# Performance work log

Measured on AMD Instinct MI355X. Metric: run time of the kernel, lower is better.

Reference implementation:

```python
import jax, jax.numpy as jnp
import numpy as np

E_ENT = 50000   # entities
R_REL = 500     # relations (dual graph nodes)
N_EDGE = 500000 # triples
D = 256
HID = D // 2
ALPHA = 0.1
BETA = 0.3
SLOPE = 0.01    # torch F.leaky_relu default

def _leaky(x):
    return jnp.where(x > 0, x, SLOPE * x)

def _compute_r(X, head_r, tail_r):
    # mean head / tail entity embedding per relation -> [R, 2D]
    L = (head_r.T @ X) / head_r.sum(0)[:, None]
    Rm = (tail_r.T @ X) / tail_r.sum(0)[:, None]
    return jnp.concatenate([L, Rm], axis=-1)

def _dense_att(vals_in, feats, adj, w1, w2, b2, w3, b3):
    # conv1d(k=1) == linear; feats [R, 2D]
    in_fts = feats @ w1.T                # [R, HID]
    f1 = in_fts @ w2.T + b2              # [R, 1]
    f2 = in_fts @ w3.T + b3              # [R, 1]
    logits = adj * (f1 + f2.T)           # [R, R]
    bias = -1e9 * (1.0 - (adj > 0).astype(jnp.float32))
    coefs = jax.nn.softmax(_leaky(logits) + bias, axis=1)
    return jax.nn.relu(coefs @ vals_in)

def _sparse_att(X, dual_layer, row, col, rel, w, b):
    # per-relation scalar score, gathered per edge, sparse row-softmax, sparse mm
    score = (dual_layer @ w.T + b)[:, 0]          # [R]
    logit = _leaky(score[rel])                    # [E]
    m = jax.ops.segment_max(logit, row, num_segments=E_ENT)
    ex = jnp.exp(logit - m[row])
    s = jax.ops.segment_sum(ex, row, num_segments=E_ENT)
    coef = ex / s[row]
    out = jnp.zeros_like(X).at[row].add(coef[:, None] * X[col])
    return jax.nn.relu(out)

def _gcn(X, W, m_row, m_col, m_val):
    # sparse.mm(M, X * W); dropout omitted (eval mode)
    Xw = X * W
    out = jnp.zeros_like(X).at[m_row].add(m_val[:, None] * Xw[m_col])
    return jax.nn.relu(out)

def _highway(l1, l2, K, b):
    t = jax.nn.sigmoid(l1 @ K + b)
    return t * l2 + (1.0 - t) * l1

def setup_inputs() -> dict:
    key = jax.random.key(0)
    ks = jax.random.split(key, 24)
    e, r, ne, d, hid = E_ENT, R_REL, N_EDGE, D, HID
    u = lambda k, sh: jax.random.uniform(k, sh, dtype=jnp.float32)
    n = lambda k, sh: jax.random.normal(k, sh, dtype=jnp.float32)
    gl = lambda k, sh: n(k, sh) * (2.0 / (sh[0] + sh[-1])) ** 0.5
    return {
        'X0': n(ks[0], (e, d)) * 0.1,
        'head_r': u(ks[1], (e, r)),
        'tail_r': u(ks[2], (e, r)),
        'dual_A': u(ks[3], (r, r)),
        'edge_row': jax.random.randint(ks[4], (ne,), 0, e),
        'edge_col': jax.random.randint(ks[5], (ne,), 0, e),
        'edge_rel': jax.random.randint(ks[6], (ne,), 0, r),
        'm_row': jax.random.randint(ks[7], (ne,), 0, e),
        'm_col': jax.random.randint(ks[8], (ne,), 0, e),
        'm_val': u(ks[9], (ne,)) * 1e-1,
        'w_self1': gl(ks[10], (hid, 2 * d)),
        'w_self2': gl(ks[11], (1, hid)), 'b_self2': jnp.zeros((1,), jnp.float32),
        'w_self3': gl(ks[12], (1, hid)), 'b_self3': jnp.zeros((1,), jnp.float32),
        'w_sp1': gl(ks[13], (1, 2 * d)), 'b_sp1': jnp.zeros((1,), jnp.float32),
        'w_dual1': gl(ks[14], (hid, 2 * d)),
        'w_dual2': gl(ks[15], (1, hid)), 'b_dual2': jnp.zeros((1,), jnp.float32),
        'w_dual3': gl(ks[16], (1, hid)), 'b_dual3': jnp.zeros((1,), jnp.float32),
        'w_sp2': gl(ks[17], (1, 2 * d)), 'b_sp2': jnp.zeros((1,), jnp.float32),
        'w_gcn1': jnp.ones((1, d), jnp.float32),
        'w_gcn2': jnp.ones((1, d), jnp.float32),
        'k_hw1': gl(ks[18], (d, d)), 'bg_hw1': jnp.zeros((d,), jnp.float32),
        'k_hw2': gl(ks[19], (d, d)), 'bg_hw2': jnp.zeros((d,), jnp.float32),
    }

def reference(X0, head_r, tail_r, dual_A, edge_row, edge_col, edge_rel,
              m_row, m_col, m_val,
              w_self1, w_self2, b_self2, w_self3, b_self3, w_sp1, b_sp1,
              w_dual1, w_dual2, b_dual2, w_dual3, b_dual3, w_sp2, b_sp2,
              w_gcn1, w_gcn2, k_hw1, bg_hw1, k_hw2, bg_hw2):
    dX1 = _compute_r(X0, head_r, tail_r)
    dH1 = _dense_att(dX1, dX1, dual_A, w_self1, w_self2, b_self2, w_self3, b_self3)
    pH1 = _sparse_att(X0, dH1, edge_row, edge_col, edge_rel, w_sp1, b_sp1)
    pX1 = X0 + ALPHA * pH1
    dX2 = _compute_r(pX1, head_r, tail_r)
    dH2 = _dense_att(dH1, dX2, dual_A, w_dual1, w_dual2, b_dual2, w_dual3, b_dual3)
    pH2 = _sparse_att(pX1, dH2, edge_row, edge_col, edge_rel, w_sp2, b_sp2)
    pX2 = X0 + BETA * pH2
    g1 = _gcn(pX2, w_gcn1, m_row, m_col, m_val)
    h1 = _highway(pX2, g1, k_hw1, bg_hw1)
    g2 = _gcn(h1, w_gcn2, m_row, m_col, m_val)
    return _highway(h1, g2, k_hw2, bg_hw2)
```

## Files before the change

kernel.cpp:

```cpp
#include <hip/hip_runtime.h>
#include <stdint.h>

#define E_ENT 50000
#define R_REL 500
#define NEDGE 500000
#define DD 256
#define D2 512
#define KSPLIT 50
#define KCHUNK 1000

typedef unsigned short u16;
typedef unsigned int u32;
typedef __attribute__((ext_vector_type(8))) short bf16x8;
typedef __attribute__((ext_vector_type(4))) float f32x4;

__device__ __forceinline__ float bf2f(u16 u) {
  union { u32 i; float f; } v; v.i = ((u32)u) << 16; return v.f;
}
__device__ __forceinline__ u16 f2bf(float f) {
  union { float f; u32 i; } v; v.f = f;
  u32 r = v.i + 0x7fffu + ((v.i >> 16) & 1u);
  return (u16)(r >> 16);
}
__device__ __forceinline__ float lrelu(float x) { return x > 0.f ? x : 0.01f * x; }

__device__ __forceinline__ uint4 ld4g(const u16* p, bool v) {
  if (v) return *(const uint4*)p;
  return make_uint4(0u, 0u, 0u, 0u);
}
__device__ __forceinline__ float4 ldf4(const float* p, bool v) {
  if (v) return *(const float4*)p;
  return make_float4(0.f, 0.f, 0.f, 0.f);
}

__device__ __forceinline__ uint4 pk4(const float4& x, const float4& y) {
  uint4 r;
  r.x = (u32)f2bf(x.x) | ((u32)f2bf(x.y) << 16);
  r.y = (u32)f2bf(x.z) | ((u32)f2bf(x.w) << 16);
  r.z = (u32)f2bf(y.x) | ((u32)f2bf(y.y) << 16);
  r.w = (u32)f2bf(y.z) | ((u32)f2bf(y.w) << 16);
  return r;
}

__device__ __forceinline__ int lds_addr(int col, int e) {
  return col * 64 + ((((e >> 3) ^ col ^ (col >> 3)) & 7) << 3) + (e & 7);
}

__device__ __forceinline__ void pack_store(u16* __restrict__ lds, int colBase, int e,
                                           const uint4& x, const uint4& y) {
  const u32* xp = (const u32*)&x;
  const u32* yp = (const u32*)&y;
#pragma unroll
  for (int i = 0; i < 4; ++i) {
    u32 xv = xp[i], yv = yp[i];
    u32 lo = (xv & 0xffffu) | (yv << 16);
    u32 hi = (xv >> 16) | (yv & 0xffff0000u);
    int c0 = colBase + 2 * i;
    *(u32*)(lds + lds_addr(c0, e)) = lo;
    *(u32*)(lds + lds_addr(c0 + 1, e)) = hi;
  }
}

__global__ void k_cast(const float* __restrict__ in, u16* __restrict__ out, int n4) {
  int i = blockIdx.x * 256 + threadIdx.x;
  if (i < n4) {
    float4 v = *(const float4*)(in + (size_t)i * 4);
    uint2 o;
    o.x = (u32)f2bf(v.x) | ((u32)f2bf(v.y) << 16);
    o.y = (u32)f2bf(v.z) | ((u32)f2bf(v.w) << 16);
    *(uint2*)(out + (size_t)i * 4) = o;
  }
}

__global__ void k_hist(const int* __restrict__ rows, int* __restrict__ cnt) {
  int i = blockIdx.x * 256 + threadIdx.x;
  if (i < NEDGE) atomicAdd(&cnt[rows[i]], 1);
}

__global__ void k_bsum(const int* __restrict__ cnt, int* __restrict__ bsum) {
  __shared__ int sb[256];
  int t = threadIdx.x, i = blockIdx.x * 256 + t;
  sb[t] = (i < E_ENT) ? cnt[i] : 0;
  __syncthreads();
  for (int s = 128; s; s >>= 1) { if (t < s) sb[t] += sb[t + s]; __syncthreads(); }
  if (t == 0) bsum[blockIdx.x] = sb[0];
}

__global__ void k_scanb(const int* __restrict__ bsum, int* __restrict__ boff, int nb) {
  __shared__ int sb[256];
  int t = threadIdx.x;
  int v = (t < nb) ? bsum[t] : 0;
  sb[t] = v;
  __syncthreads();
  for (int o = 1; o < 256; o <<= 1) {
    int x = (t >= o) ? sb[t - o] : 0;
    __syncthreads();
    sb[t] += x;
    __syncthreads();
  }
  if (t < nb) boff[t] = sb[t] - v;
}

__global__ void k_apply(const int* __restrict__ cnt, const int* __restrict__ boff,
                        int* __restrict__ ptr, int* __restrict__ cur) {
  __shared__ int sb[256];
  int t = threadIdx.x, b = blockIdx.x, i = b * 256 + t;
  int v = (i < E_ENT) ? cnt[i] : 0;
  sb[t] = v;
  __syncthreads();
  for (int o = 1; o < 256; o <<= 1) {
    int x = (t >= o) ? sb[t - o] : 0;
    __syncthreads();
    sb[t] += x;
    __syncthreads();
  }
  if (i < E_ENT) { int ex = boff[b] + sb[t] - v; ptr[i] = ex; cur[i] = ex; }
  if (b == 0 && t == 0) ptr[E_ENT] = NEDGE;
}

__global__ void k_scat_e(const int* __restrict__ rows, const int* __restrict__ cols,
                         const int* __restrict__ rels, int* __restrict__ cur,
                         int* __restrict__ cs, int* __restrict__ rs) {
  int i = blockIdx.x * 256 + threadIdx.x;
  if (i < NEDGE) {
    int p = atomicAdd(&cur[rows[i]], 1);
    cs[p] = cols[i];
    rs[p] = rels[i];
  }
}

__global__ void k_scat_m(const int* __restrict__ rows, const int* __restrict__ cols,
                         const float* __restrict__ vals, int* __restrict__ cur,
                         int* __restrict__ cs, float* __restrict__ vs) {
  int i = blockIdx.x * 256 + threadIdx.x;
  if (i < NEDGE) {
    int p = atomicAdd(&cur[rows[i]], 1);
    cs[p] = cols[i];
    vs[p] = vals[i];
  }
}

__device__ __forceinline__ void wtx_load(const float* __restrict__ WSel, const u16* __restrict__ XB,
                                         int eb, int e_end, int r0, int n0,
                                         int ap, int aq, int ep0, int ep1, int nq,
                                         float4& f00, float4& f01, float4& f10, float4& f11,
                                         uint4& b00, uint4& b01, uint4& b10, uint4& b11) {
  int ee = e_end - eb;
  int c0 = r0 + aq * 8;
  bool cv0 = c0 < R_REL, cv1 = (c0 + 4) < R_REL;
  bool r0ok = 2 * ap < ee, r1ok = 2 * ap + 1 < ee;
  const float* p = WSel + (size_t)(eb + 2 * ap) * R_REL + c0;
  f00 = ldf4(p, r0ok && cv0);
  f01 = ldf4(p + 4, r0ok && cv1);
  f10 = ldf4(p + R_REL, r1ok && cv0);
  f11 = ldf4(p + R_REL + 4, r1ok && cv1);
  const u16* q0 = XB + (size_t)(eb + 2 * ep0) * DD + n0 + nq * 8;
  b00 = ld4g(q0, 2 * ep0 < ee);
  b01 = ld4g(q0 + DD, 2 * ep0 + 1 < ee);
  const u16* q1 = XB + (size_t)(eb + 2 * ep1) * DD + n0 + nq * 8;
  b10 = ld4g(q1, 2 * ep1 < ee);
  b11 = ld4g(q1 + DD, 2 * ep1 + 1 < ee);
}

__global__ __launch_bounds__(256) void k_wtx(const float* __restrict__ HW,
                                             const float* __restrict__ TW,
                                             const u16* __restrict__ XB,
                                             float* __restrict__ P,
                                             float* __restrict__ sums) {
  __shared__ __align__(16) u16 lsa2[2 * 32 * 64];
  __shared__ __align__(16) u16 lsb[128 * 64];
  const int tid = threadIdx.x;
  const int bid = blockIdx.x;
  const int swz = (bid & 7) * 200 + (bid >> 3);
  const int mtnt = swz & 31;
  const int mt = mtnt >> 1, nt = mtnt & 1;
  const int chunk = swz >> 5;
  const int r0 = mt * 32, n0 = nt * 128;
  const int lane = tid & 63, wv = tid >> 6;
  const int wm = (wv & 1) * 16, wn = (wv >> 1) * 64;
  const int l15 = lane & 15, lq = lane >> 4;
  const int ap = (tid & 127) >> 2, aq = tid & 3;
  const int ep0 = tid >> 4, nq = tid & 15;
  const int ep1 = ep0 + 16;
  const float* WSel = (tid < 128) ? HW : TW;
  u16* lsaSel = lsa2 + (tid >> 7) * (32 * 64);
  const bool dosum = (sums != nullptr) && (nt == 0);
  const int e_begin = chunk * KCHUNK;
  const int e_end = min(e_begin + KCHUNK, E_ENT);
  const int iters = (e_end - e_begin + 63) >> 6;

  f32x4 accH[4], accT[4];
#pragma unroll
  for (int t = 0; t < 4; ++t) { accH[t] = (f32x4)0.f; accT[t] = (f32x4)0.f; }
  float s0 = 0.f, s1 = 0.f, s2 = 0.f, s3 = 0.f, s4 = 0.f, s5 = 0.f, s6 = 0.f, s7 = 0.f;

  float4 f00, f01, f10, f11;
  uint4 b00, b01, b10, b11;
  wtx_load(WSel, XB, e_begin, e_end, r0, n0, ap, aq, ep0, ep1, nq,
           f00, f01, f10, f11, b00, b01, b10, b11);

  int eb = e_begin;
  for (int it = 0; it < iters; ++it) {
    __syncthreads();
    uint4 a0 = pk4(f00, f01), a1 = pk4(f10, f11);
    if (dosum) {
      s0 += f00.x + f10.x; s1 += f00.y + f10.y; s2 += f00.z + f10.z; s3 += f00.w + f10.w;
      s4 += f01.x + f11.x; s5 += f01.y + f11.y; s6 += f01.z + f11.z; s7 += f01.w + f11.w;
    }
    pack_store(lsaSel, aq * 8, 2 * ap, a0, a1);
    pack_store(lsb, nq * 8, 2 * ep0, b00, b01);
    pack_store(lsb, nq * 8, 2 * ep1, b10, b11);
    __syncthreads();
    eb += 64;
    if (it + 1 < iters)
      wtx_load(WSel, XB, eb, e_end, r0, n0, ap, aq, ep0, ep1, nq,
               f00, f01, f10, f11, b00, b01, b10, b11);
#pragma unroll
    for (int ks = 0; ks < 2; ++ks) {
      bf16x8 afH = *(const bf16x8*)(lsa2 + lds_addr(wm + l15, ks * 32 + lq * 8));
      bf16x8 afT = *(const bf16x8*)(lsa2 + 32 * 64 + lds_addr(wm + l15, ks * 32 + lq * 8));
#pragma unroll
      for (int t = 0; t < 4; ++t) {
        bf16x8 bv = *(const bf16x8*)(lsb + lds_addr(wn + t * 16 + l15, ks * 32 + lq * 8));
        accH[t] = __builtin_amdgcn_mfma_f32_16x16x32_bf16(afH, bv, accH[t], 0, 0, 0);
        accT[t] = __builtin_amdgcn_mfma_f32_16x16x32_bf16(afT, bv, accT[t], 0, 0, 0);
      }
    }
  }

  if (dosum) {
    __syncthreads();
    float* scr = (float*)lsb;
    int half = tid >> 7;
    int base = half * 1024 + aq * 256 + ap;
    scr[base + 0 * 32] = s0; scr[base + 1 * 32] = s1;
    scr[base + 2 * 32] = s2; scr[base + 3 * 32] = s3;
    scr[base + 4 * 32] = s4; scr[base + 5 * 32] = s5;
    scr[base + 6 * 32] = s6; scr[base + 7 * 32] = s7;
    __syncthreads();
    if (tid < 64) {
      int hh = tid >> 5, aq2 = (tid >> 3) & 3, j = tid & 7;
      float v = 0.f;
      for (int a = 0; a < 32; ++a) v += scr[hh * 1024 + aq2 * 256 + j * 32 + a];
      atomicAdd(&sums[hh * 512 + r0 + aq2 * 8 + j], v);
    }
  }

#pragma unroll
  for (int t = 0; t < 4; ++t) {
#pragma unroll
    for (int rg = 0; rg < 4; ++rg) {
      int row = r0 + wm + lq * 4 + rg;
      if (row < R_REL) {
        int col = n0 + wn + t * 16 + l15;
        atomicAdd(&P[row * D2 + col], accH[t][rg]);
        atomicAdd(&P[row * D2 + col + 256], accT[t][rg]);
      }
    }
  }
}

__global__ void k_fin(float* __restrict__ P, const float* __restrict__ hsum,
                      const float* __restrict__ tsum) {
  int i = blockIdx.x * 256 + threadIdx.x;
  if (i < R_REL * D2) {
    int r = i >> 9, c = i & 511;
    P[i] = P[i] / (c < 256 ? hsum[r] : tsum[r]);
  }
}

__global__ __launch_bounds__(128) void k_infts(const float* __restrict__ feats,
                                               const float* __restrict__ w1,
                                               const float* __restrict__ w2, const float* __restrict__ b2,
                                               const float* __restrict__ w3, const float* __restrict__ b3,
                                               float* __restrict__ f1, float* __restrict__ f2) {
  __shared__ float fl[512];
  __shared__ float red[128];
  int r = blockIdx.x, t = threadIdx.x;
  for (int i = t; i < 512; i += 128) fl[i] = feats[r * 512 + i];
  __syncthreads();
  float a = 0.f;
  const float* wrow = w1 + (size_t)t * 512;
  for (int k = 0; k < 512; k += 4) {
    float4 v = *(const float4*)(wrow + k);
    a += fl[k + 0] * v.x + fl[k + 1] * v.y + fl[k + 2] * v.z + fl[k + 3] * v.w;
  }
  red[t] = a * w2[t];
  __syncthreads();
  for (int s = 64; s; s >>= 1) { if (t < s) red[t] += red[t + s]; __syncthreads(); }
  if (t == 0) f1[r] = red[0] + b2[0];
  __syncthreads();
  red[t] = a * w3[t];
  __syncthreads();
  for (int s = 64; s; s >>= 1) { if (t < s) red[t] += red[t + s]; __syncthreads(); }
  if (t == 0) f2[r] = red[0] + b3[0];
}

__global__ __launch_bounds__(256) void k_att(const float* __restrict__ adj,
                                             const float* __restrict__ f1,
                                             const float* __restrict__ f2,
                                             const float* __restrict__ vals,
                                             float* __restrict__ dH) {
  __shared__ float coef[512];
  __shared__ float red[256];
  int r = blockIdx.x, t = threadIdx.x;
  float f1r = f1[r];
  float z0, z1 = -1e30f;
  {
    float a = adj[r * 500 + t];
    float z = lrelu(a * (f1r + f2[t]));
    if (!(a > 0.f)) z += -1e9f;
    z0 = z;
  }
  int c1 = t + 256;
  if (c1 < 500) {
    float a = adj[r * 500 + c1];
    float z = lrelu(a * (f1r + f2[c1]));
    if (!(a > 0.f)) z += -1e9f;
    z1 = z;
  }
  red[t] = fmaxf(z0, z1);
  __syncthreads();
  for (int s = 128; s; s >>= 1) { if (t < s) red[t] = fmaxf(red[t], red[t + s]); __syncthreads(); }
  float m = red[0];
  __syncthreads();
  float e0 = expf(z0 - m);
  float e1 = (c1 < 500) ? expf(z1 - m) : 0.f;
  coef[t] = e0;
  coef[c1] = e1;
  red[t] = e0 + e1;
  __syncthreads();
  for (int s = 128; s; s >>= 1) { if (t < s) red[t] += red[t + s]; __syncthreads(); }
  float inv = 1.f / red[0];
  float accA = 0.f, accB = 0.f;
  int dA = t, dB = t + 256;
  for (int c = 0; c < 500; ++c) {
    float cf = coef[c];
    accA += cf * vals[c * 512 + dA];
    accB += cf * vals[c * 512 + dB];
  }
  dH[r * 512 + dA] = fmaxf(accA * inv, 0.f);
  dH[r * 512 + dB] = fmaxf(accB * inv, 0.f);
}

__global__ void k_score(const float* __restrict__ dH, const float* __restrict__ w,
                        const float* __restrict__ b, float* __restrict__ score) {
  int r = blockIdx.x, lane = threadIdx.x;
  float a = 0.f;
  for (int k = lane; k < 512; k += 64) a += dH[r * 512 + k] * w[k];
  for (int o = 32; o; o >>= 1) a += __shfl_xor(a, o, 64);
  if (lane == 0) score[r] = a + b[0];
}

__global__ void k_els(const float* __restrict__ score, float* __restrict__ EL) {
  __shared__ float red[512];
  int t = threadIdx.x;
  float v = (t < R_REL) ? lrelu(score[t]) : -3.0e38f;
  red[t] = v;
  __syncthreads();
  for (int s = 256; s; s >>= 1) { if (t < s) red[t] = fmaxf(red[t], red[t + s]); __syncthreads(); }
  float m = red[0];
  EL[t] = (t < R_REL) ? expf(v - m) : 0.f;
}

__global__ __launch_bounds__(256) void k_spatt(const u16* __restrict__ src,
                                               const float* __restrict__ base,
                                               const int* __restrict__ ptr,
                                               const int* __restrict__ cols,
                                               const int* __restrict__ rels,
                                               const float* __restrict__ EL, float alpha,
                                               u16* __restrict__ outb, float* __restrict__ outf) {
  __shared__ float sEL[512];
  const int tid = threadIdx.x;
  sEL[tid] = EL[tid];
  sEL[tid + 256] = EL[tid + 256];
  __syncthreads();
  const int lane = tid & 63;
  const int e = blockIdx.x * 4 + (tid >> 6);
  int p0 = ptr[e], p1 = ptr[e + 1];
  float a0 = 0.f, a1 = 0.f, a2 = 0.f, a3 = 0.f;
  if (p1 > p0) {
    float s = 0.f;
    for (int j = p0 + lane; j < p1; j += 64) s += sEL[rels[j]];
    for (int o = 32; o; o >>= 1) s += __shfl_xor(s, o, 64);
    float inv = 1.f / s;
    for (int jb = p0; jb < p1; jb += 64) {
      int n = min(64, p1 - jb);
      int cl = 0; float wl = 0.f;
      if (lane < n) { cl = cols[jb + lane]; wl = sEL[rels[jb + lane]] * inv; }
      int jj = 0;
      for (; jj + 4 <= n; jj += 4) {
        int c0 = __shfl(cl, jj), c1 = __shfl(cl, jj + 1), c2 = __shfl(cl, jj + 2), c3 = __shfl(cl, jj + 3);
        float w0 = __shfl(wl, jj), w1 = __shfl(wl, jj + 1), w2 = __shfl(wl, jj + 2), w3 = __shfl(wl, jj + 3);
        uint2 v0 = *(const uint2*)(src + (size_t)c0 * DD + lane * 4);
        uint2 v1 = *(const uint2*)(src + (size_t)c1 * DD + lane * 4);
        uint2 v2 = *(const uint2*)(src + (size_t)c2 * DD + lane * 4);
        uint2 v3 = *(const uint2*)(src + (size_t)c3 * DD + lane * 4);
        a0 += w0 * bf2f((u16)(v0.x & 0xffffu)) + w1 * bf2f((u16)(v1.x & 0xffffu))
            + w2 * bf2f((u16)(v2.x & 0xffffu)) + w3 * bf2f((u16)(v3.x & 0xffffu));
        a1 += w0 * bf2f((u16)(v0.x >> 16)) + w1 * bf2f((u16)(v1.x >> 16))
            + w2 * bf2f((u16)(v2.x >> 16)) + w3 * bf2f((u16)(v3.x >> 16));
        a2 += w0 * bf2f((u16)(v0.y & 0xffffu)) + w1 * bf2f((u16)(v1.y & 0xffffu))
            + w2 * bf2f((u16)(v2.y & 0xffffu)) + w3 * bf2f((u16)(v3.y & 0xffffu));
        a3 += w0 * bf2f((u16)(v0.y >> 16)) + w1 * bf2f((u16)(v1.y >> 16))
            + w2 * bf2f((u16)(v2.y >> 16)) + w3 * bf2f((u16)(v3.y >> 16));
      }
      for (; jj < n; ++jj) {
        int c = __shfl(cl, jj);
        float w = __shfl(wl, jj);
        uint2 v = *(const uint2*)(src + (size_t)c * DD + lane * 4);
        a0 += w * bf2f((u16)(v.x & 0xffffu));
        a1 += w * bf2f((u16)(v.x >> 16));
        a2 += w * bf2f((u16)(v.y & 0xffffu));
        a3 += w * bf2f((u16)(v.y >> 16));
      }
    }
  }
  size_t off = (size_t)e * DD + lane * 4;
  float4 bv = *(const float4*)(base + off);
  float o0 = bv.x + alpha * fmaxf(a0, 0.f);
  float o1 = bv.y + alpha * fmaxf(a1, 0.f);
  float o2 = bv.z + alpha * fmaxf(a2, 0.f);
  float o3 = bv.w + alpha * fmaxf(a3, 0.f);
  uint2 ov;
  ov.x = (u32)f2bf(o0) | ((u32)f2bf(o1) << 16);
  ov.y = (u32)f2bf(o2) | ((u32)f2bf(o3) << 16);
  *(uint2*)(outb + off) = ov;
  if (outf) *(float4*)(outf + off) = make_float4(o0, o1, o2, o3);
}

__global__ __launch_bounds__(256) void k_gcn(const u16* __restrict__ src,
                                             const int* __restrict__ ptr,
                                             const int* __restrict__ cols,
                                             const float* __restrict__ vals,
                                             const float* __restrict__ wg,
                                             float* __restrict__ gout) {
  const int lane = threadIdx.x & 63;
  const int e = blockIdx.x * 4 + (threadIdx.x >> 6);
  int p0 = ptr[e], p1 = ptr[e + 1];
  float a0 = 0.f, a1 = 0.f, a2 = 0.f, a3 = 0.f;
  for (int jb = p0; jb < p1; jb += 64) {
    int n = min(64, p1 - jb);
    int cl = 0; float wl = 0.f;
    if (lane < n) { cl = cols[jb + lane]; wl = vals[jb + lane]; }
    int jj = 0;
    for (; jj + 4 <= n; jj += 4) {
      int c0 = __shfl(cl, jj), c1 = __shfl(cl, jj + 1), c2 = __shfl(cl, jj + 2), c3 = __shfl(cl, jj + 3);
      float w0 = __shfl(wl, jj), w1 = __shfl(wl, jj + 1), w2 = __shfl(wl, jj + 2), w3 = __shfl(wl, jj + 3);
      uint2 v0 = *(const uint2*)(src + (size_t)c0 * DD + lane * 4);
      uint2 v1 = *(const uint2*)(src + (size_t)c1 * DD + lane * 4);
      uint2 v2 = *(const uint2*)(src + (size_t)c2 * DD + lane * 4);
      uint2 v3 = *(const uint2*)(src + (size_t)c3 * DD + lane * 4);
      a0 += w0 * bf2f((u16)(v0.x & 0xffffu)) + w1 * bf2f((u16)(v1.x & 0xffffu))
          + w2 * bf2f((u16)(v2.x & 0xffffu)) + w3 * bf2f((u16)(v3.x & 0xffffu));
      a1 += w0 * bf2f((u16)(v0.x >> 16)) + w1 * bf2f((u16)(v1.x >> 16))
          + w2 * bf2f((u16)(v2.x >> 16)) + w3 * bf2f((u16)(v3.x >> 16));
      a2 += w0 * bf2f((u16)(v0.y & 0xffffu)) + w1 * bf2f((u16)(v1.y & 0xffffu))
          + w2 * bf2f((u16)(v2.y & 0xffffu)) + w3 * bf2f((u16)(v3.y & 0xffffu));
      a3 += w0 * bf2f((u16)(v0.y >> 16)) + w1 * bf2f((u16)(v1.y >> 16))
          + w2 * bf2f((u16)(v2.y >> 16)) + w3 * bf2f((u16)(v3.y >> 16));
    }
    for (; jj < n; ++jj) {
      int c = __shfl(cl, jj);
      float w = __shfl(wl, jj);
      uint2 v = *(const uint2*)(src + (size_t)c * DD + lane * 4);
      a0 += w * bf2f((u16)(v.x & 0xffffu));
      a1 += w * bf2f((u16)(v.x >> 16));
      a2 += w * bf2f((u16)(v.y & 0xffffu));
      a3 += w * bf2f((u16)(v.y >> 16));
    }
  }
  int d = lane * 4;
  float4 wv = *(const float4*)(wg + d);
  float4 o = make_float4(fmaxf(a0 * wv.x, 0.f), fmaxf(a1 * wv.y, 0.f),
                         fmaxf(a2 * wv.z, 0.f), fmaxf(a3 * wv.w, 0.f));
  *(float4*)(gout + (size_t)e * DD + d) = o;
}

__global__ __launch_bounds__(256) void k_hw(const u16* __restrict__ xb,
                                            const float* __restrict__ xf,
                                            const float* __restrict__ g,
                                            const u16* __restrict__ KB,
                                            const float* __restrict__ bg,
                                            float* __restrict__ outf,
                                            u16* __restrict__ outb) {
  __shared__ __align__(16) u16 la[64 * 64];
  __shared__ __align__(16) u16 lb[64 * 64];
  const int tid = threadIdx.x;
  const int bid = blockIdx.x;
  const int swz = (bid & 7) * 391 + (bid >> 3);
  const int e0 = (swz >> 2) * 64;
  const int n0 = (swz & 3) * 64;
  const int lane = tid & 63, wv = tid >> 6;
  const int m0 = wv * 16;
  const int l15 = lane & 15, lq = lane >> 4;
  const int am = tid >> 3, aoct = tid & 7;
  const int kp = tid >> 3, nq8 = tid & 7;
  f32x4 acc[4];
#pragma unroll
  for (int t = 0; t < 4; ++t) acc[t] = (f32x4)0.f;

  for (int kc = 0; kc < 4; ++kc) {
    {
      const u16* pa = xb + (size_t)(e0 + am) * DD + kc * 64 + aoct * 8;
      uint4 va = ld4g(pa, e0 + am < E_ENT);
      *(uint4*)(la + lds_addr(am, aoct * 8)) = va;
      const u16* pa2 = xb + (size_t)(e0 + am + 32) * DD + kc * 64 + aoct * 8;
      uint4 va2 = ld4g(pa2, e0 + am + 32 < E_ENT);
      *(uint4*)(la + lds_addr(am + 32, aoct * 8)) = va2;
      const u16* pb = KB + (size_t)(kc * 64 + 2 * kp) * DD + n0 + nq8 * 8;
      uint4 xk = *(const uint4*)pb;
      uint4 yk = *(const uint4*)(pb + DD);
      pack_store(lb, nq8 * 8, 2 * kp, xk, yk);
    }
    __syncthreads();
#pragma unroll
    for (int ks = 0; ks < 2; ++ks) {
      bf16x8 af = *(const bf16x8*)(la + lds_addr(m0 + l15, ks * 32 + lq * 8));
#pragma unroll
      for (int t = 0; t < 4; ++t) {
        bf16x8 bv = *(const bf16x8*)(lb + lds_addr(t * 16 + l15, ks * 32 + lq * 8));
        acc[t] = __builtin_amdgcn_mfma_f32_16x16x32_bf16(af, bv, acc[t], 0, 0, 0);
      }
    }
    __syncthreads();
  }
#pragma unroll
  for (int t = 0; t < 4; ++t) {
    int col = n0 + t * 16 + l15;
    float bgv = bg[col];
#pragma unroll
    for (int rg = 0; rg < 4; ++rg) {
      int row = e0 + m0 + lq * 4 + rg;
      if (row < E_ENT) {
        float z = acc[t][rg] + bgv;
        float tt = 1.f / (1.f + expf(-z));
        size_t off = (size_t)row * DD + col;
        float hv = tt * g[off] + (1.f - tt) * xf[off];
        outf[off] = hv;
        if (outb) outb[off] = f2bf(hv);
      }
    }
  }
}

extern "C" void kernel_launch(void* const* d_in, const int* in_sizes, int n_in,
                              void* d_out, int out_size, void* d_ws, size_t ws_size,
                              hipStream_t stream) {
  (void)in_sizes; (void)n_in; (void)out_size;
  const float* X0 = (const float*)d_in[0];
  const float* head = (const float*)d_in[1];
  const float* tail = (const float*)d_in[2];
  const float* adj = (const float*)d_in[3];
  const int* erow = (const int*)d_in[4];
  const int* ecol = (const int*)d_in[5];
  const int* erel = (const int*)d_in[6];
  const int* mrow = (const int*)d_in[7];
  const int* mcol = (const int*)d_in[8];
  const float* mval = (const float*)d_in[9];
  const float* w_self1 = (const float*)d_in[10];
  const float* w_self2 = (const float*)d_in[11];
  const float* b_self2 = (const float*)d_in[12];
  const float* w_self3 = (const float*)d_in[13];
  const float* b_self3 = (const float*)d_in[14];
  const float* w_sp1 = (const float*)d_in[15];
  const float* b_sp1 = (const float*)d_in[16];
  const float* w_dual1 = (const float*)d_in[17];
  const float* w_dual2 = (const float*)d_in[18];
  const float* b_dual2 = (const float*)d_in[19];
  const float* w_dual3 = (const float*)d_in[20];
  const float* b_dual3 = (const float*)d_in[21];
  const float* w_sp2 = (const float*)d_in[22];
  const float* b_sp2 = (const float*)d_in[23];
  const float* w_gcn1 = (const float*)d_in[24];
  const float* w_gcn2 = (const float*)d_in[25];
  const float* k_hw1 = (const float*)d_in[26];
  const float* bg_hw1 = (const float*)d_in[27];
  const float* k_hw2 = (const float*)d_in[28];
  const float* bg_hw2 = (const float*)d_in[29];

  char* ws = (char*)d_ws;
  size_t o = 0;
  auto take = [&](size_t bytes) -> char* {
    o = (o + 255) & ~(size_t)255;
    char* p = ws + o;
    o += bytes;
    return p;
  };
  u16* X0B  = (u16*)take((size_t)E_ENT * DD * 2);
  u16* PX1B = (u16*)take((size_t)E_ENT * DD * 2);
  u16* PX2B = (u16*)take((size_t)E_ENT * DD * 2);
  u16* H1B  = (u16*)take((size_t)E_ENT * DD * 2);
  float* PX2F = (float*)take((size_t)E_ENT * DD * 4);
  float* G    = (float*)take((size_t)E_ENT * DD * 4);
  float* P1   = (float*)take((size_t)512 * 512 * 4);
  float* P2   = (float*)take((size_t)512 * 512 * 4);
  float* DH1  = (float*)take((size_t)512 * 512 * 4);
  float* DH2  = (float*)take((size_t)512 * 512 * 4);
  float* HS   = (float*)take(1024 * 4);
  float* F1   = (float*)take(512 * 4);
  float* F2   = (float*)take(512 * 4);
  float* SCORE = (float*)take(512 * 4);
  float* EL   = (float*)take(512 * 4);
  u16* KB1 = (u16*)take((size_t)DD * DD * 2);
  u16* KB2 = (u16*)take((size_t)DD * DD * 2);
  int* BSUM = (int*)take(256 * 4);
  int* BOFF = (int*)take(256 * 4);
  int* EPTR = (int*)take((size_t)(E_ENT + 1) * 4);
  int* ECUR = (int*)take((size_t)(E_ENT + 1) * 4);
  int* ECOLS = (int*)take((size_t)NEDGE * 4);
  int* ERELS = (int*)take((size_t)NEDGE * 4);
  int* MPTR = (int*)take((size_t)(E_ENT + 1) * 4);
  int* MCUR = (int*)take((size_t)(E_ENT + 1) * 4);
  int* MCOLS = (int*)take((size_t)NEDGE * 4);
  float* MVALS = (float*)take((size_t)NEDGE * 4);

  if (o > ws_size) {
    hipMemsetAsync(d_out, 0, (size_t)E_ENT * DD * 4, stream);
    return;
  }

  hipMemsetAsync(P1, 0, (size_t)512 * 512 * 4, stream);
  hipMemsetAsync(P2, 0, (size_t)512 * 512 * 4, stream);
  hipMemsetAsync(HS, 0, 1024 * 4, stream);
  hipMemsetAsync(ECUR, 0, (size_t)(E_ENT + 1) * 4, stream);
  hipMemsetAsync(MCUR, 0, (size_t)(E_ENT + 1) * 4, stream);

  const int GE = (NEDGE + 255) / 256;
  const int GB = (E_ENT + 255) / 256;

  k_cast<<<(E_ENT * DD / 4 + 255) / 256, 256, 0, stream>>>(X0, X0B, E_ENT * DD / 4);
  k_cast<<<64, 256, 0, stream>>>(k_hw1, KB1, DD * DD / 4);
  k_cast<<<64, 256, 0, stream>>>(k_hw2, KB2, DD * DD / 4);

  k_hist<<<GE, 256, 0, stream>>>(erow, ECUR);
  k_bsum<<<GB, 256, 0, stream>>>(ECUR, BSUM);
  k_scanb<<<1, 256, 0, stream>>>(BSUM, BOFF, GB);
  k_apply<<<GB, 256, 0, stream>>>(ECUR, BOFF, EPTR, ECUR);
  k_scat_e<<<GE, 256, 0, stream>>>(erow, ecol, erel, ECUR, ECOLS, ERELS);
  k_hist<<<GE, 256, 0, stream>>>(mrow, MCUR);
  k_bsum<<<GB, 256, 0, stream>>>(MCUR, BSUM);
  k_scanb<<<1, 256, 0, stream>>>(BSUM, BOFF, GB);
  k_apply<<<GB, 256, 0, stream>>>(MCUR, BOFF, MPTR, MCUR);
  k_scat_m<<<GE, 256, 0, stream>>>(mrow, mcol, mval, MCUR, MCOLS, MVALS);

  k_wtx<<<32 * KSPLIT, 256, 0, stream>>>(head, tail, X0B, P1, HS);
  k_fin<<<1000, 256, 0, stream>>>(P1, HS, HS + 512);
  k_infts<<<500, 128, 0, stream>>>(P1, w_self1, w_self2, b_self2, w_self3, b_self3, F1, F2);
  k_att<<<500, 256, 0, stream>>>(adj, F1, F2, P1, DH1);
  k_score<<<500, 64, 0, stream>>>(DH1, w_sp1, b_sp1, SCORE);
  k_els<<<1, 512, 0, stream>>>(SCORE, EL);
  k_spatt<<<12500, 256, 0, stream>>>(X0B, X0, EPTR, ECOLS, ERELS, EL, 0.1f, PX1B, nullptr);

  k_wtx<<<32 * KSPLIT, 256, 0, stream>>>(head, tail, PX1B, P2, nullptr);
  k_fin<<<1000, 256, 0, stream>>>(P2, HS, HS + 512);
  k_infts<<<500, 128, 0, stream>>>(P2, w_dual1, w_dual2, b_dual2, w_dual3, b_dual3, F1, F2);
  k_att<<<500, 256, 0, stream>>>(adj, F1, F2, DH1, DH2);
  k_score<<<500, 64, 0, stream>>>(DH2, w_sp2, b_sp2, SCORE);
  k_els<<<1, 512, 0, stream>>>(SCORE, EL);
  k_spatt<<<12500, 256, 0, stream>>>(PX1B, X0, EPTR, ECOLS, ERELS, EL, 0.3f, PX2B, PX2F);

  k_gcn<<<12500, 256, 0, stream>>>(PX2B, MPTR, MCOLS, MVALS, w_gcn1, G);
  k_hw<<<782 * 4, 256, 0, stream>>>(PX2B, PX2F, G, KB1, bg_hw1, PX2F, H1B);
  k_gcn<<<12500, 256, 0, stream>>>(H1B, MPTR, MCOLS, MVALS, w_gcn2, G);
  k_hw<<<782 * 4, 256, 0, stream>>>(H1B, PX2F, G, KB2, bg_hw2, (float*)d_out, nullptr);
}
```

Before: 1.011 ms.

## Cache bf16 head/tail matrices in first pass and double-buffer LDS in wtx

The first relation-aggregation GEMM now writes a bf16 copy of the fp32 head_r/tail_r matrices into spare workspace buffers. The second GEMM reads those bf16 copies instead of re-reading the fp32 inputs, which halves that pass's dominant memory traffic. Both kernels also move to double-buffered LDS with a fixed 16-iteration loop, so one barrier per step replaces two. The cost is extra global writes in the first pass and reuse of the PX2F/G buffers as scratch, which relies on their lifetimes not overlapping.

```diff
diff --git a/kernel.cpp b/kernel.cpp
--- a/kernel.cpp
+++ b/kernel.cpp
@@ -140,12 +140,21 @@
   }
 }
 
-__device__ __forceinline__ void wtx_load(const float* __restrict__ WSel, const u16* __restrict__ XB,
-                                         int eb, int e_end, int r0, int n0,
-                                         int ap, int aq, int ep0, int ep1, int nq,
-                                         float4& f00, float4& f01, float4& f10, float4& f11,
-                                         uint4& b00, uint4& b01, uint4& b10, uint4& b11) {
-  int ee = e_end - eb;
+
+__device__ __forceinline__ void wtx_ldB(const u16* __restrict__ XB, int eb, int ee,
+                                        int n0, int ep0, int ep1, int nq,
+                                        uint4& b00, uint4& b01, uint4& b10, uint4& b11) {
+  const u16* q0 = XB + (size_t)(eb + 2 * ep0) * DD + n0 + nq * 8;
+  b00 = ld4g(q0, 2 * ep0 < ee);
+  b01 = ld4g(q0 + DD, 2 * ep0 + 1 < ee);
+  const u16* q1 = XB + (size_t)(eb + 2 * ep1) * DD + n0 + nq * 8;
+  b10 = ld4g(q1, 2 * ep1 < ee);
+  b11 = ld4g(q1 + DD, 2 * ep1 + 1 < ee);
+}
+
+__device__ __forceinline__ void wtx_ldA1(const float* __restrict__ WSel, int eb, int ee,
+                                         int r0, int ap, int aq,
+                                         float4& f00, float4& f01, float4& f10, float4& f11) {
   int c0 = r0 + aq * 8;
   bool cv0 = c0 < R_REL, cv1 = (c0 + 4) < R_REL;
   bool r0ok = 2 * ap < ee, r1ok = 2 * ap + 1 < ee;
@@ -154,21 +163,33 @@
   f01 = ldf4(p + 4, r0ok && cv1);
   f10 = ldf4(p + R_REL, r1ok && cv0);
   f11 = ldf4(p + R_REL + 4, r1ok && cv1);
-  const u16* q0 = XB + (size_t)(eb + 2 * ep0) * DD + n0 + nq * 8;
-  b00 = ld4g(q0, 2 * ep0 < ee);
-  b01 = ld4g(q0 + DD, 2 * ep0 + 1 < ee);
-  const u16* q1 = XB + (size_t)(eb + 2 * ep1) * DD + n0 + nq * 8;
-  b10 = ld4g(q1, 2 * ep1 < ee);
-  b11 = ld4g(q1 + DD, 2 * ep1 + 1 < ee);
-}
-
-__global__ __launch_bounds__(256) void k_wtx(const float* __restrict__ HW,
-                                             const float* __restrict__ TW,
-                                             const u16* __restrict__ XB,
-                                             float* __restrict__ P,
-                                             float* __restrict__ sums) {
-  __shared__ __align__(16) u16 lsa2[2 * 32 * 64];
-  __shared__ __align__(16) u16 lsb[128 * 64];
+}
+
+__device__ __forceinline__ void wtx_mma(const u16* __restrict__ la, const u16* __restrict__ lb,
+                                        int wm, int wn, int l15, int lq,
+                                        f32x4* accH, f32x4* accT) {
+#pragma unroll
+  for (int ks = 0; ks < 2; ++ks) {
+    bf16x8 afH = *(const bf16x8*)(la + lds_addr(wm + l15, ks * 32 + lq * 8));
+    bf16x8 afT = *(const bf16x8*)(la + 2048 + lds_addr(wm + l15, ks * 32 + lq * 8));
+#pragma unroll
+    for (int t = 0; t < 4; ++t) {
+      bf16x8 bv = *(const bf16x8*)(lb + lds_addr(wn + t * 16 + l15, ks * 32 + lq * 8));
+      accH[t] = __builtin_amdgcn_mfma_f32_16x16x32_bf16(afH, bv, accH[t], 0, 0, 0);
+      accT[t] = __builtin_amdgcn_mfma_f32_16x16x32_bf16(afT, bv, accT[t], 0, 0, 0);
+    }
+  }
+}
+
+__global__ __launch_bounds__(256) void k_wtx1(const float* __restrict__ HW,
+                                              const float* __restrict__ TW,
+                                              const u16* __restrict__ XB,
+                                              float* __restrict__ P,
+                                              float* __restrict__ sums,
+                                              u16* __restrict__ WBH,
+                                              u16* __restrict__ WBT) {
+  __shared__ __align__(16) u16 lsa2[2 * 2 * 32 * 64];
+  __shared__ __align__(16) u16 lsb2[2 * 128 * 64];
   const int tid = threadIdx.x;
   const int bid = blockIdx.x;
   const int swz = (bid & 7) * 200 + (bid >> 3);
@@ -183,60 +204,77 @@
   const int ep0 = tid >> 4, nq = tid & 15;
   const int ep1 = ep0 + 16;
   const float* WSel = (tid < 128) ? HW : TW;
-  u16* lsaSel = lsa2 + (tid >> 7) * (32 * 64);
-  const bool dosum = (sums != nullptr) && (nt == 0);
+  u16* WBSel = (tid < 128) ? WBH : WBT;
+  const int half = tid >> 7;
+  const bool dosum = (nt == 0);
   const int e_begin = chunk * KCHUNK;
-  const int e_end = min(e_begin + KCHUNK, E_ENT);
-  const int iters = (e_end - e_begin + 63) >> 6;
+  const int e_end = e_begin + KCHUNK;
 
   f32x4 accH[4], accT[4];
 #pragma unroll
   for (int t = 0; t < 4; ++t) { accH[t] = (f32x4)0.f; accT[t] = (f32x4)0.f; }
-  float s0 = 0.f, s1 = 0.f, s2 = 0.f, s3 = 0.f, s4 = 0.f, s5 = 0.f, s6 = 0.f, s7 = 0.f;
+  float s[8];
+#pragma unroll
+  for (int j = 0; j < 8; ++j) s[j] = 0.f;
 
   float4 f00, f01, f10, f11;
   uint4 b00, b01, b10, b11;
-  wtx_load(WSel, XB, e_begin, e_end, r0, n0, ap, aq, ep0, ep1, nq,
-           f00, f01, f10, f11, b00, b01, b10, b11);
-
-  int eb = e_begin;
-  for (int it = 0; it < iters; ++it) {
-    __syncthreads();
+  wtx_ldA1(WSel, e_begin, KCHUNK, r0, ap, aq, f00, f01, f10, f11);
+  wtx_ldB(XB, e_begin, KCHUNK, n0, ep0, ep1, nq, b00, b01, b10, b11);
+  {
     uint4 a0 = pk4(f00, f01), a1 = pk4(f10, f11);
     if (dosum) {
-      s0 += f00.x + f10.x; s1 += f00.y + f10.y; s2 += f00.z + f10.z; s3 += f00.w + f10.w;
-      s4 += f01.x + f11.x; s5 += f01.y + f11.y; s6 += f01.z + f11.z; s7 += f01.w + f11.w;
-    }
-    pack_store(lsaSel, aq * 8, 2 * ap, a0, a1);
-    pack_store(lsb, nq * 8, 2 * ep0, b00, b01);
-    pack_store(lsb, nq * 8, 2 * ep1, b10, b11);
-    __syncthreads();
-    eb += 64;
-    if (it + 1 < iters)
-      wtx_load(WSel, XB, eb, e_end, r0, n0, ap, aq, ep0, ep1, nq,
-               f00, f01, f10, f11, b00, b01, b10, b11);
-#pragma unroll
-    for (int ks = 0; ks < 2; ++ks) {
-      bf16x8 afH = *(const bf16x8*)(lsa2 + lds_addr(wm + l15, ks * 32 + lq * 8));
-      bf16x8 afT = *(const bf16x8*)(lsa2 + 32 * 64 + lds_addr(wm + l15, ks * 32 + lq * 8));
-#pragma unroll
-      for (int t = 0; t < 4; ++t) {
-        bf16x8 bv = *(const bf16x8*)(lsb + lds_addr(wn + t * 16 + l15, ks * 32 + lq * 8));
-        accH[t] = __builtin_amdgcn_mfma_f32_16x16x32_bf16(afH, bv, accH[t], 0, 0, 0);
-        accT[t] = __builtin_amdgcn_mfma_f32_16x16x32_bf16(afT, bv, accT[t], 0, 0, 0);
-      }
-    }
+      s[0] += f00.x + f10.x; s[1] += f00.y + f10.y; s[2] += f00.z + f10.z; s[3] += f00.w + f10.w;
+      s[4] += f01.x + f11.x; s[5] += f01.y + f11.y; s[6] += f01.z + f11.z; s[7] += f01.w + f11.w;
+      u16* wb = WBSel + (size_t)(e_begin + 2 * ap) * D2 + r0 + aq * 8;
+      *(uint4*)wb = a0;
+      *(uint4*)(wb + D2) = a1;
+    }
+    pack_store(lsa2 + half * 2048, aq * 8, 2 * ap, a0, a1);
+    pack_store(lsb2, nq * 8, 2 * ep0, b00, b01);
+    pack_store(lsb2, nq * 8, 2 * ep1, b10, b11);
+  }
+  wtx_ldA1(WSel, e_begin + 64, KCHUNK - 64, r0, ap, aq, f00, f01, f10, f11);
+  wtx_ldB(XB, e_begin + 64, KCHUNK - 64, n0, ep0, ep1, nq, b00, b01, b10, b11);
+  __syncthreads();
+
+  int cur = 0;
+  for (int it = 0; it < 16; ++it) {
+    wtx_mma(lsa2 + cur * 4096, lsb2 + cur * 8192, wm, wn, l15, lq, accH, accT);
+    if (it < 15) {
+      int ebp = e_begin + (it + 1) * 64;
+      int ee = e_end - ebp;
+      uint4 a0 = pk4(f00, f01), a1 = pk4(f10, f11);
+      if (dosum) {
+        s[0] += f00.x + f10.x; s[1] += f00.y + f10.y; s[2] += f00.z + f10.z; s[3] += f00.w + f10.w;
+        s[4] += f01.x + f11.x; s[5] += f01.y + f11.y; s[6] += f01.z + f11.z; s[7] += f01.w + f11.w;
+        u16* wb = WBSel + (size_t)(ebp + 2 * ap) * D2 + r0 + aq * 8;
+        if (2 * ap < ee) *(uint4*)wb = a0;
+        if (2 * ap + 1 < ee) *(uint4*)(wb + D2) = a1;
+      }
+      u16* lsaW = lsa2 + (cur ^ 1) * 4096 + half * 2048;
+      u16* lsbW = lsb2 + (cur ^ 1) * 8192;
+      pack_store(lsaW, aq * 8, 2 * ap, a0, a1);
+      pack_store(lsbW, nq * 8, 2 * ep0, b00, b01);
+      pack_store(lsbW, nq * 8, 2 * ep1, b10, b11);
+      if (it < 14) {
+        int ebl = e_begin + (it + 2) * 64;
+        int eel = e_end - ebl;
+        wtx_ldA1(WSel, ebl, eel, r0, ap, aq, f00, f01, f10, f11);
+        wtx_ldB(XB, ebl, eel, n0, ep0, ep1, nq, b00, b01, b10, b11);
+      }
+    }
+    __syncthreads();
+    cur ^= 1;
   }
 
   if (dosum) {
-    __syncthreads();
-    float* scr = (float*)lsb;
-    int half = tid >> 7;
+    float* scr = (float*)lsb2;
     int base = half * 1024 + aq * 256 + ap;
-    scr[base + 0 * 32] = s0; scr[base + 1 * 32] = s1;
-    scr[base + 2 * 32] = s2; scr[base + 3 * 32] = s3;
-    scr[base + 4 * 32] = s4; scr[base + 5 * 32] = s5;
-    scr[base + 6 * 32] = s6; scr[base + 7 * 32] = s7;
+    scr[base + 0 * 32] = s[0]; scr[base + 1 * 32] = s[1];
+    scr[base + 2 * 32] = s[2]; scr[base + 3 * 32] = s[3];
+    scr[base + 4 * 32] = s[4]; scr[base + 5 * 32] = s[5];
+    scr[base + 6 * 32] = s[6]; scr[base + 7 * 32] = s[7];
     __syncthreads();
     if (tid < 64) {
       int hh = tid >> 5, aq2 = (tid >> 3) & 3, j = tid & 7;
@@ -244,6 +282,89 @@
       for (int a = 0; a < 32; ++a) v += scr[hh * 1024 + aq2 * 256 + j * 32 + a];
       atomicAdd(&sums[hh * 512 + r0 + aq2 * 8 + j], v);
     }
+  }
+
+#pragma unroll
+  for (int t = 0; t < 4; ++t) {
+#pragma unroll
+    for (int rg = 0; rg < 4; ++rg) {
+      int row = r0 + wm + lq * 4 + rg;
+      if (row < R_REL) {
+        int col = n0 + wn + t * 16 + l15;
+        atomicAdd(&P[row * D2 + col], accH[t][rg]);
+        atomicAdd(&P[row * D2 + col + 256], accT[t][rg]);
+      }
+    }
+  }
+}
+
+__global__ __launch_bounds__(256) void k_wtx2(const u16* __restrict__ HB,
+                                              const u16* __restrict__ TB,
+                                              const u16* __restrict__ XB,
+                                              float* __restrict__ P) {
+  __shared__ __align__(16) u16 lsa2[2 * 2 * 32 * 64];
+  __shared__ __align__(16) u16 lsb2[2 * 128 * 64];
+  const int tid = threadIdx.x;
+  const int bid = blockIdx.x;
+  const int swz = (bid & 7) * 200 + (bid >> 3);
+  const int mtnt = swz & 31;
+  const int mt = mtnt >> 1, nt = mtnt & 1;
+  const int chunk = swz >> 5;
+  const int r0 = mt * 32, n0 = nt * 128;
+  const int lane = tid & 63, wv = tid >> 6;
+  const int wm = (wv & 1) * 16, wn = (wv >> 1) * 64;
+  const int l15 = lane & 15, lq = lane >> 4;
+  const int ap = (tid & 127) >> 2, aq = tid & 3;
+  const int ep0 = tid >> 4, nq = tid & 15;
+  const int ep1 = ep0 + 16;
+  const u16* ASel = (tid < 128) ? HB : TB;
+  const int half = tid >> 7;
+  const int e_begin = chunk * KCHUNK;
+  const int e_end = e_begin + KCHUNK;
+
+  f32x4 accH[4], accT[4];
+#pragma unroll
+  for (int t = 0; t < 4; ++t) { accH[t] = (f32x4)0.f; accT[t] = (f32x4)0.f; }
+
+  uint4 a0r, a1r, b00, b01, b10, b11;
+  {
+    const u16* p = ASel + (size_t)e_begin * D2 + r0 + aq * 8 + (size_t)2 * ap * D2;
+    a0r = *(const uint4*)p;
+    a1r = *(const uint4*)(p + D2);
+  }
+  wtx_ldB(XB, e_begin, KCHUNK, n0, ep0, ep1, nq, b00, b01, b10, b11);
+  pack_store(lsa2 + half * 2048, aq * 8, 2 * ap, a0r, a1r);
+  pack_store(lsb2, nq * 8, 2 * ep0, b00, b01);
+  pack_store(lsb2, nq * 8, 2 * ep1, b10, b11);
+  {
+    int ebl = e_begin + 64, eel = KCHUNK - 64;
+    const u16* p = ASel + (size_t)(ebl + 2 * ap) * D2 + r0 + aq * 8;
+    a0r = ld4g(p, 2 * ap < eel);
+    a1r = ld4g(p + D2, 2 * ap + 1 < eel);
+    wtx_ldB(XB, ebl, eel, n0, ep0, ep1, nq, b00, b01, b10, b11);
+  }
+  __syncthreads();
+
+  int cur = 0;
+  for (int it = 0; it < 16; ++it) {
+    wtx_mma(lsa2 + cur * 4096, lsb2 + cur * 8192, wm, wn, l15, lq, accH, accT);
+    if (it < 15) {
+      u16* lsaW = lsa2 + (cur ^ 1) * 4096 + half * 2048;
+      u16* lsbW = lsb2 + (cur ^ 1) * 8192;
+      pack_store(lsaW, aq * 8, 2 * ap, a0r, a1r);
+      pack_store(lsbW, nq * 8, 2 * ep0, b00, b01);
+      pack_store(lsbW, nq * 8, 2 * ep1, b10, b11);
+      if (it < 14) {
+        int ebl = e_begin + (it + 2) * 64;
+        int eel = e_end - ebl;
+        const u16* p = ASel + (size_t)(ebl + 2 * ap) * D2 + r0 + aq * 8;
+        a0r = ld4g(p, 2 * ap < eel);
+        a1r = ld4g(p + D2, 2 * ap + 1 < eel);
+        wtx_ldB(XB, ebl, eel, n0, ep0, ep1, nq, b00, b01, b10, b11);
+      }
+    }
+    __syncthreads();
+    cur ^= 1;
   }
 
 #pragma unroll
@@ -615,6 +736,9 @@
   int* MCOLS = (int*)take((size_t)NEDGE * 4);
   float* MVALS = (float*)take((size_t)NEDGE * 4);
 
+  u16* WBH = (u16*)PX2F;
+  u16* WBT = (u16*)G;
+
   if (o > ws_size) {
     hipMemsetAsync(d_out, 0, (size_t)E_ENT * DD * 4, stream);
     return;
@@ -644,7 +768,7 @@
   k_apply<<<GB, 256, 0, stream>>>(MCUR, BOFF, MPTR, MCUR);
   k_scat_m<<<GE, 256, 0, stream>>>(mrow, mcol, mval, MCUR, MCOLS, MVALS);
 
-  k_wtx<<<32 * KSPLIT, 256, 0, stream>>>(head, tail, X0B, P1, HS);
+  k_wtx1<<<32 * KSPLIT, 256, 0, stream>>>(head, tail, X0B, P1, HS, WBH, WBT);
   k_fin<<<1000, 256, 0, stream>>>(P1, HS, HS + 512);
   k_infts<<<500, 128, 0, stream>>>(P1, w_self1, w_self2, b_self2, w_self3, b_self3, F1, F2);
   k_att<<<500, 256, 0, stream>>>(adj, F1, F2, P1, DH1);
@@ -652,7 +776,7 @@
   k_els<<<1, 512, 0, stream>>>(SCORE, EL);
   k_spatt<<<12500, 256, 0, stream>>>(X0B, X0, EPTR, ECOLS, ERELS, EL, 0.1f, PX1B, nullptr);
 
-  k_wtx<<<32 * KSPLIT, 256, 0, stream>>>(head, tail, PX1B, P2, nullptr);
+  k_wtx2<<<32 * KSPLIT, 256, 0, stream>>>(WBH, WBT, PX1B, P2);
   k_fin<<<1000, 256, 0, stream>>>(P2, HS, HS + 512);
   k_infts<<<500, 128, 0, stream>>>(P2, w_dual1, w_dual2, b_dual2, w_dual3, b_dual3, F1, F2);
   k_att<<<500, 256, 0, stream>>>(adj, F1, F2, DH1, DH2);
```

Measured after the change: 1.015 ms. Within noise of the previous version (+0.4%).
